# Optimization experiments

Hardware: AMD Instinct MI355X
Metric: run time of the kernel (lower is better)

The kernel has to match this reference:

```python
import jax, jax.numpy as jnp
import numpy as np

N = 50000   # nodes
E = 800000  # edges (before self-loops)
IN = 128    # input feature dim
H = 4       # attention heads


def setup_inputs() -> dict:
    key = jax.random.key(0)
    ks = jax.random.split(key, 32)
    f = lambda k, s: (jax.random.normal(k, s, dtype=jnp.float32) * 0.1)
    inp = {
        "x": jax.random.normal(ks[0], (N, IN), dtype=jnp.float32),
        "edge_index": jax.random.randint(ks[1], (2, E), 0, N, dtype=jnp.int32),
        "edge_attr": jax.random.normal(ks[2], (E, 1), dtype=jnp.float32),
        # GATConv 1: 128 -> 8 per head, 4 heads (concat -> 32)
        "W1": f(ks[3], (IN, 32)), "as1": f(ks[4], (H, 8)), "ad1": f(ks[5], (H, 8)), "b1": jnp.zeros((32,), jnp.float32),
        # GATConv 2: 32 -> 16 per head (concat -> 64)
        "W2": f(ks[6], (32, 64)), "as2": f(ks[7], (H, 16)), "ad2": f(ks[8], (H, 16)), "b2": jnp.zeros((64,), jnp.float32),
        # GATConv 3: 64 -> 32 per head (concat -> 128)
        "W3": f(ks[9], (64, 128)), "as3": f(ks[10], (H, 32)), "ad3": f(ks[11], (H, 32)), "b3": jnp.zeros((128,), jnp.float32),
        # GATConv 4: 128 -> 64 per head (concat -> 256)
        "W4": f(ks[12], (128, 256)), "as4": f(ks[13], (H, 64)), "ad4": f(ks[14], (H, 64)), "b4": jnp.zeros((256,), jnp.float32),
        # MLP head
        "Wr": f(ks[15], (256, 32)), "br": jnp.zeros((32,), jnp.float32),
        "Wf1": f(ks[16], (32, 64)), "bf1": jnp.zeros((64,), jnp.float32),
        "Wf2": f(ks[17], (64, 1)), "bf2": jnp.zeros((1,), jnp.float32),
    }
    return inp


def _gat_layer(x, W, a_src, a_dst, bias, src, dst):
    """PyG GATConv (concat=True, negative_slope=0.2, self-loops appended upstream)."""
    heads, C = a_src.shape
    h = (x @ W).reshape(-1, heads, C)              # [N, H, C]
    alpha_s = jnp.sum(h * a_src[None], axis=-1)    # [N, H]
    alpha_d = jnp.sum(h * a_dst[None], axis=-1)    # [N, H]
    e = jax.nn.leaky_relu(alpha_s[src] + alpha_d[dst], 0.2)  # [E', H]
    # segment softmax over incoming edges of each destination node
    emax = jax.ops.segment_max(e, dst, num_segments=N)
    ee = jnp.exp(e - emax[dst])
    denom = jax.ops.segment_sum(ee, dst, num_segments=N)
    alpha = ee / denom[dst]                        # [E', H]
    msg = h[src] * alpha[:, :, None]               # [E', H, C]
    out = jax.ops.segment_sum(msg, dst, num_segments=N)  # [N, H, C]
    return out.reshape(-1, heads * C) + bias


def reference(x, edge_index, edge_attr,
              W1, as1, ad1, b1, W2, as2, ad2, b2,
              W3, as3, ad3, b3, W4, as4, ad4, b4,
              Wr, br, Wf1, bf1, Wf2, bf2):
    # edge_attr is accepted but unused, matching the original forward.
    loop = jnp.arange(N, dtype=edge_index.dtype)
    src = jnp.concatenate([edge_index[0], loop])   # add self-loops (PyG default)
    dst = jnp.concatenate([edge_index[1], loop])
    h = jax.nn.elu(_gat_layer(x, W1, as1, ad1, b1, src, dst))
    h = jax.nn.elu(_gat_layer(h, W2, as2, ad2, b2, src, dst))
    h = jax.nn.elu(_gat_layer(h, W3, as3, ad3, b3, src, dst))
    h = jax.nn.elu(_gat_layer(h, W4, as4, ad4, b4, src, dst))
    h = jax.nn.elu(h @ Wr + br)
    h = jax.nn.elu(h @ Wf1 + bf1)
    return h @ Wf2 + bf2                           # [N, 1]
```

## Files before the change

kernel.cpp:

```cpp
#include <hip/hip_runtime.h>
#include <hip/hip_fp16.h>
#include <math.h>

constexpr int NN = 50000;
constexpr int NE = 800000;
constexpr int NEP = NE + NN;
constexpr int CAP = 96;
constexpr int SCAT_B = (NEP + 255) / 256;

typedef _Float16 half8_t __attribute__((ext_vector_type(8)));
typedef float    f32x4_t __attribute__((ext_vector_type(4)));

__device__ __forceinline__ float lrelu02(float x) { return x > 0.f ? x : 0.2f * x; }
__device__ __forceinline__ float eluf(float x)    { return x > 0.f ? x : (__expf(x) - 1.f); }
__device__ __forceinline__ float pick4(float4 q, int hd) {
  return (hd == 0) ? q.x : (hd == 1) ? q.y : (hd == 2) ? q.z : q.w;
}


__device__ __forceinline__ void pack_w_one(const float* __restrict__ W,
                                           __half* __restrict__ Wp,
                                           int M, int tid, int total) {
  if (tid >= total) return;
  int CT = M >> 4;
  int l = tid & 63;
  int c = (tid >> 6) % CT;
  int kc = (tid >> 6) / CT;
  int n = l & 15, q = l >> 4;
  __half* dst = Wp + (size_t)tid * 8;
  const float* src = W + (size_t)(kc * 32 + q * 8) * M + c * 16 + n;
  #pragma unroll
  for (int j = 0; j < 8; j++) dst[j] = __float2half_rn(src[j * M]);
}


__global__ __launch_bounds__(256) void scatter_pack_kernel(
    const int* __restrict__ edge_src, const int* __restrict__ edge_dst,
    int* __restrict__ count, int* __restrict__ csr_src,
    const float* __restrict__ W1, __half* __restrict__ Wp1,
    const float* __restrict__ W2, __half* __restrict__ Wp2,
    const float* __restrict__ W3, __half* __restrict__ Wp3,
    const float* __restrict__ W4, __half* __restrict__ Wp4,
    const float* __restrict__ Wr, __half* __restrict__ Wrp,
    const float* __restrict__ Wf1, __half* __restrict__ Wf1p) {
  int b = blockIdx.x;
  if (b < SCAT_B) {
    int i = b * 256 + threadIdx.x;
    if (i < NEP) {
      int s, d;
      if (i < NE) { s = edge_src[i]; d = edge_dst[i]; } else { s = i - NE; d = s; }
      int pos = atomicAdd(&count[d], 1);
      if (pos < CAP) csr_src[d * CAP + pos] = s;
    }
  } else {
    int tid = (b - SCAT_B) * 256 + threadIdx.x;
    if (tid < 512)            pack_w_one(W1, Wp1, 32,  tid,        512);
    else if (tid < 768)       pack_w_one(W2, Wp2, 64,  tid - 512,  256);
    else if (tid < 1792)      pack_w_one(W3, Wp3, 128, tid - 768,  1024);
    else if (tid < 5888)      pack_w_one(W4, Wp4, 256, tid - 1792, 4096);
    else if (tid < 6912)      pack_w_one(Wr, Wrp, 32,  tid - 5888, 1024);
    else if (tid < 7168)      pack_w_one(Wf1, Wf1p, 64, tid - 6912, 256);
  }
}


template<int M, int C, int CT>
__device__ __forceinline__ void alpha_epilogue(const f32x4_t* acc,
    const float* __restrict__ a_src, const float* __restrict__ a_dst,
    int row_base, int m, float* __restrict__ as_out, float* __restrict__ ad_out) {
  float aS[CT], aD[CT];
  #pragma unroll
  for (int c = 0; c < CT; c++) { aS[c] = a_src[c * 16 + m]; aD[c] = a_dst[c * 16 + m]; }

  if constexpr (C == 8) {
    #pragma unroll
    for (int r = 0; r < 4; r++) {
      float p0 = acc[0][r] * aS[0], p1 = acc[1][r] * aS[1];
      float q0 = acc[0][r] * aD[0], q1 = acc[1][r] * aD[1];
      #pragma unroll
      for (int off = 1; off < 8; off <<= 1) {
        p0 += __shfl_xor(p0, off); p1 += __shfl_xor(p1, off);
        q0 += __shfl_xor(q0, off); q1 += __shfl_xor(q1, off);
      }
      int row = row_base + r;
      if ((m & 7) == 0 && row < NN) {
        int hb = m >> 3;
        as_out[row * 4 + hb]     = p0;
        as_out[row * 4 + 2 + hb] = p1;
        ad_out[row * 4 + hb]     = q0;
        ad_out[row * 4 + 2 + hb] = q1;
      }
    }
  } else {
    constexpr int FPH = C / 16;
    #pragma unroll
    for (int r = 0; r < 4; r++) {
      float bs[4] = {0.f, 0.f, 0.f, 0.f}, bd[4] = {0.f, 0.f, 0.f, 0.f};
      #pragma unroll
      for (int c = 0; c < CT; c++) {
        int hd = c / FPH;
        bs[hd] += acc[c][r] * aS[c];
        bd[hd] += acc[c][r] * aD[c];
      }
      #pragma unroll
      for (int off = 1; off < 16; off <<= 1)
        #pragma unroll
        for (int h = 0; h < 4; h++) {
          bs[h] += __shfl_xor(bs[h], off);
          bd[h] += __shfl_xor(bd[h], off);
        }
      int row = row_base + r;
      if (m < 4 && row < NN) {
        float vs = (m == 0) ? bs[0] : (m == 1) ? bs[1] : (m == 2) ? bs[2] : bs[3];
        float vd = (m == 0) ? bd[0] : (m == 1) ? bd[1] : (m == 2) ? bd[2] : bd[3];
        as_out[row * 4 + m] = vs;
        ad_out[row * 4 + m] = vd;
      }
    }
  }
}


template<int M, int K, int C>
__global__ __launch_bounds__(256) void gemm_mfma_f32_kernel(const float* __restrict__ A,
    const __half* __restrict__ Wp, __half* __restrict__ Ch,
    const float* __restrict__ a_src, const float* __restrict__ a_dst,
    float* __restrict__ as_out, float* __restrict__ ad_out) {
  constexpr int CT = M / 16;
  constexpr int KC = K / 32;
  __shared__ _Float16 Ah[64 * 40];
  int t = threadIdx.x;
  int w = t >> 6, l = t & 63;
  int m = l & 15, q = l >> 4;
  int row0 = blockIdx.x * 64;

  f32x4_t acc[CT];
  #pragma unroll
  for (int c = 0; c < CT; c++) acc[c] = (f32x4_t){0.f, 0.f, 0.f, 0.f};

  const half8_t* Bfrag = (const half8_t*)Wp;

  for (int kc = 0; kc < KC; kc++) {
    __syncthreads();
    #pragma unroll
    for (int i = 0; i < 2; i++) {
      int idx = t + 256 * i;
      int row = idx >> 3, c4 = idx & 7;
      int gr = row0 + row; if (gr >= NN) gr = NN - 1;
      float4 v = *(const float4*)(A + (size_t)gr * K + kc * 32 + c4 * 4);
      _Float16 h[4] = {(_Float16)v.x, (_Float16)v.y, (_Float16)v.z, (_Float16)v.w};
      *(uint2*)(&Ah[row * 40 + c4 * 4]) = *(const uint2*)h;
    }
    __syncthreads();
    half8_t a = *(const half8_t*)(&Ah[(w * 16 + m) * 40 + q * 8]);
    #pragma unroll
    for (int c = 0; c < CT; c++) {
      half8_t b = Bfrag[(kc * CT + c) * 64 + l];
      acc[c] = __builtin_amdgcn_mfma_f32_16x16x32_f16(a, b, acc[c], 0, 0, 0);
    }
  }

  #pragma unroll
  for (int r = 0; r < 4; r++) {
    int row = row0 + w * 16 + q * 4 + r;
    if (row < NN) {
      #pragma unroll
      for (int c = 0; c < CT; c++)
        Ch[(size_t)row * M + c * 16 + m] = __float2half_rn(acc[c][r]);
    }
  }
  alpha_epilogue<M, C, CT>(acc, a_src, a_dst, row0 + w * 16 + q * 4, m, as_out, ad_out);
}


template<int M, int K, int C>
__global__ __launch_bounds__(256) void gemm_mfma_f16_kernel(const __half* __restrict__ A,
    const __half* __restrict__ Wp, __half* __restrict__ Ch,
    const float* __restrict__ a_src, const float* __restrict__ a_dst,
    float* __restrict__ as_out, float* __restrict__ ad_out) {
  constexpr int CT = M / 16;
  constexpr int KC = K / 32;
  __shared__ _Float16 Ah[64 * 40];
  int t = threadIdx.x;
  int w = t >> 6, l = t & 63;
  int m = l & 15, q = l >> 4;
  int row0 = blockIdx.x * 64;

  f32x4_t acc[CT];
  #pragma unroll
  for (int c = 0; c < CT; c++) acc[c] = (f32x4_t){0.f, 0.f, 0.f, 0.f};

  const half8_t* Bfrag = (const half8_t*)Wp;

  for (int kc = 0; kc < KC; kc++) {
    __syncthreads();
    {
      int row = t >> 2, c8 = t & 3;
      int gr = row0 + row; if (gr >= NN) gr = NN - 1;
      uint4 v = *(const uint4*)(A + (size_t)gr * K + kc * 32 + c8 * 8);
      *(uint4*)(&Ah[row * 40 + c8 * 8]) = v;
    }
    __syncthreads();
    half8_t a = *(const half8_t*)(&Ah[(w * 16 + m) * 40 + q * 8]);
    #pragma unroll
    for (int c = 0; c < CT; c++) {
      half8_t b = Bfrag[(kc * CT + c) * 64 + l];
      acc[c] = __builtin_amdgcn_mfma_f32_16x16x32_f16(a, b, acc[c], 0, 0, 0);
    }
  }

  #pragma unroll
  for (int r = 0; r < 4; r++) {
    int row = row0 + w * 16 + q * 4 + r;
    if (row < NN) {
      #pragma unroll
      for (int c = 0; c < CT; c++)
        Ch[(size_t)row * M + c * 16 + m] = __float2half_rn(acc[c][r]);
    }
  }
  alpha_epilogue<M, C, CT>(acc, a_src, a_dst, row0 + w * 16 + q * 4, m, as_out, ad_out);
}


template<int HC, int C>
__global__ __launch_bounds__(256) void agg_kernel(const __half* __restrict__ h,
    const float* __restrict__ as_v, const float* __restrict__ ad_v,
    const int* __restrict__ count, const int* __restrict__ csr_src,
    const float* __restrict__ bias, __half* __restrict__ out) {
  constexpr int V = HC / 8;
  constexpr int G = 64 / V;
  constexpr int P = 4;
  __shared__ float4 see4[4][CAP];
  __shared__ int    ssrc[4][CAP];
  int wid = threadIdx.x >> 6, lane = threadIdx.x & 63;
  int dst = blockIdx.x * 4 + wid;
  int base = dst * CAP;
  int deg = count[dst]; if (deg > CAP) deg = CAP;
  float4 ad = *(const float4*)(ad_v + dst * 4);

  float d0 = 0.f, d1 = 0.f, d2 = 0.f, d3 = 0.f;
  #pragma unroll
  for (int it = 0; it < 2; it++) {
    int j = lane + it * 64;
    if (j < deg) {
      int s = csr_src[base + j];
      float4 as = *(const float4*)(as_v + s * 4);
      float4 x = make_float4(__expf(lrelu02(as.x + ad.x)), __expf(lrelu02(as.y + ad.y)),
                             __expf(lrelu02(as.z + ad.z)), __expf(lrelu02(as.w + ad.w)));
      ssrc[wid][j] = s; see4[wid][j] = x;
      d0 += x.x; d1 += x.y; d2 += x.z; d3 += x.w;
    }
  }
  #pragma unroll
  for (int off = 32; off > 0; off >>= 1) {
    d0 += __shfl_xor(d0, off); d1 += __shfl_xor(d1, off);
    d2 += __shfl_xor(d2, off); d3 += __shfl_xor(d3, off);
  }
  float4 inv = make_float4(1.f / d0, 1.f / d1, 1.f / d2, 1.f / d3);

  int g = lane / V, v = lane % V;
  int hd = (v * 8) / C;
  float invh = pick4(inv, hd);
  int steps = (deg + G - 1) / G;
  const float4* hrows = (const float4*)h;

  float  px[P];
  float4 hv[P];
  #pragma unroll
  for (int k = 0; k < P; k++) {
    int jj = k * G + g;
    bool ok = jj < deg;
    int jc = ok ? jj : 0;
    int s = ssrc[wid][jc];
    float x = ((const float*)&see4[wid][jc])[hd];
    px[k] = ok ? x * invh : 0.f;
    hv[k] = hrows[(size_t)s * V + v];
  }

  float acc[8];
  #pragma unroll
  for (int i = 0; i < 8; i++) acc[i] = 0.f;
  int nB = (steps + P - 1) / P;
  for (int b = 1; b <= nB; b++) {
    #pragma unroll
    for (int k = 0; k < P; k++) {
      const __half2* hp = (const __half2*)&hv[k];
      float2 f0 = __half22float2(hp[0]);
      float2 f1 = __half22float2(hp[1]);
      float2 f2 = __half22float2(hp[2]);
      float2 f3 = __half22float2(hp[3]);
      float p = px[k];
      acc[0] += p * f0.x; acc[1] += p * f0.y;
      acc[2] += p * f1.x; acc[3] += p * f1.y;
      acc[4] += p * f2.x; acc[5] += p * f2.y;
      acc[6] += p * f3.x; acc[7] += p * f3.y;
      int jj = (b * P + k) * G + g;
      bool ok = jj < deg;
      int jc = ok ? jj : 0;
      int s = ssrc[wid][jc];
      float x = ((const float*)&see4[wid][jc])[hd];
      px[k] = ok ? x * invh : 0.f;
      hv[k] = hrows[(size_t)s * V + v];
    }
  }

  #pragma unroll
  for (int off = V; off < 64; off <<= 1)
    #pragma unroll
    for (int i = 0; i < 8; i++) acc[i] += __shfl_xor(acc[i], off);

  if (lane < V) {
    const float4* b4 = (const float4*)bias;
    float4 ba = b4[2 * v], bb = b4[2 * v + 1];
    _Float16 o[8];
    o[0] = (_Float16)eluf(acc[0] + ba.x); o[1] = (_Float16)eluf(acc[1] + ba.y);
    o[2] = (_Float16)eluf(acc[2] + ba.z); o[3] = (_Float16)eluf(acc[3] + ba.w);
    o[4] = (_Float16)eluf(acc[4] + bb.x); o[5] = (_Float16)eluf(acc[5] + bb.y);
    o[6] = (_Float16)eluf(acc[6] + bb.z); o[7] = (_Float16)eluf(acc[7] + bb.w);
    *(uint4*)(out + (size_t)dst * HC + v * 8) = *(const uint4*)o;
  }
}


__global__ __launch_bounds__(256) void mlp_mfma_kernel(const __half* __restrict__ h4,
    const __half* __restrict__ Wrp, const float* __restrict__ br,
    const __half* __restrict__ Wf1p, const float* __restrict__ bf1,
    const float* __restrict__ Wf2, const float* __restrict__ bf2,
    float* __restrict__ out) {
  __shared__ _Float16 rS[64 * 40];
  int t = threadIdx.x;
  int w = t >> 6, l = t & 63;
  int m = l & 15, q = l >> 4;
  int row0 = blockIdx.x * 64;
  const half8_t* Bwr  = (const half8_t*)Wrp;
  const half8_t* Bwf1 = (const half8_t*)Wf1p;

  int arow = row0 + w * 16 + m; if (arow >= NN) arow = NN - 1;
  const half8_t* Arow = (const half8_t*)(h4 + (size_t)arow * 256);
  half8_t afr[8];
  #pragma unroll
  for (int kc = 0; kc < 8; kc++) afr[kc] = Arow[kc * 4 + q];
  f32x4_t acc1[2];
  acc1[0] = (f32x4_t){0.f, 0.f, 0.f, 0.f};
  acc1[1] = (f32x4_t){0.f, 0.f, 0.f, 0.f};
  #pragma unroll
  for (int kc = 0; kc < 8; kc++) {
    acc1[0] = __builtin_amdgcn_mfma_f32_16x16x32_f16(afr[kc], Bwr[(kc * 2 + 0) * 64 + l], acc1[0], 0, 0, 0);
    acc1[1] = __builtin_amdgcn_mfma_f32_16x16x32_f16(afr[kc], Bwr[(kc * 2 + 1) * 64 + l], acc1[1], 0, 0, 0);
  }
  #pragma unroll
  for (int c = 0; c < 2; c++)
    #pragma unroll
    for (int r = 0; r < 4; r++) {
      float vv = eluf(acc1[c][r] + br[c * 16 + m]);
      rS[(w * 16 + q * 4 + r) * 40 + c * 16 + m] = (_Float16)vv;
    }
  __syncthreads();

  half8_t a2 = *(const half8_t*)(&rS[(w * 16 + m) * 40 + q * 8]);
  f32x4_t acc2[4];
  #pragma unroll
  for (int c = 0; c < 4; c++) acc2[c] = (f32x4_t){0.f, 0.f, 0.f, 0.f};
  #pragma unroll
  for (int c = 0; c < 4; c++)
    acc2[c] = __builtin_amdgcn_mfma_f32_16x16x32_f16(a2, Bwf1[c * 64 + l], acc2[c], 0, 0, 0);

  float wv[4] = {Wf2[m], Wf2[16 + m], Wf2[32 + m], Wf2[48 + m]};
  float rsum[4];
  #pragma unroll
  for (int r = 0; r < 4; r++) {
    float sr = 0.f;
    #pragma unroll
    for (int c = 0; c < 4; c++)
      sr += eluf(acc2[c][r] + bf1[c * 16 + m]) * wv[c];
    #pragma unroll
    for (int off = 1; off < 16; off <<= 1) sr += __shfl_xor(sr, off);
    rsum[r] = sr;
  }
  if (m == 0) {
    float b = bf2[0];
    #pragma unroll
    for (int r = 0; r < 4; r++) {
      int row = row0 + w * 16 + q * 4 + r;
      if (row < NN) out[row] = rsum[r] + b;
    }
  }
}


extern "C" void kernel_launch(void* const* d_in, const int* in_sizes, int n_in,
                              void* d_out, int out_size, void* d_ws, size_t ws_size,
                              hipStream_t stream) {
  const float* x   = (const float*)d_in[0];
  const int*   ei  = (const int*)d_in[1];
  const float* W1  = (const float*)d_in[3];
  const float* as1 = (const float*)d_in[4];
  const float* ad1 = (const float*)d_in[5];
  const float* b1  = (const float*)d_in[6];
  const float* W2  = (const float*)d_in[7];
  const float* as2 = (const float*)d_in[8];
  const float* ad2 = (const float*)d_in[9];
  const float* b2  = (const float*)d_in[10];
  const float* W3  = (const float*)d_in[11];
  const float* as3 = (const float*)d_in[12];
  const float* ad3 = (const float*)d_in[13];
  const float* b3  = (const float*)d_in[14];
  const float* W4  = (const float*)d_in[15];
  const float* as4 = (const float*)d_in[16];
  const float* ad4 = (const float*)d_in[17];
  const float* b4  = (const float*)d_in[18];
  const float* Wr  = (const float*)d_in[19];
  const float* br  = (const float*)d_in[20];
  const float* Wf1 = (const float*)d_in[21];
  const float* bf1 = (const float*)d_in[22];
  const float* Wf2 = (const float*)d_in[23];
  const float* bf2 = (const float*)d_in[24];
  float* out = (float*)d_out;

  char* p = (char*)d_ws;
  auto alloc = [&](size_t bytes) {
    char* q = p;
    p += (bytes + 255) & ~(size_t)255;
    return q;
  };
  int* count   = (int*)alloc((size_t)NN * 4);
  int* csr_src = (int*)alloc((size_t)NN * CAP * 4);
  __half* Hh = (__half*)alloc((size_t)NN * 256 * 2);
  __half* B2 = (__half*)alloc((size_t)NN * 128 * 2);
  __half* B3 = (__half*)alloc((size_t)NN * 256 * 2);
  float* as_buf = (float*)alloc((size_t)NN * 4 * 4);
  float* ad_buf = (float*)alloc((size_t)NN * 4 * 4);
  __half* Wp1 = (__half*)alloc((size_t)128 * 32 * 2);
  __half* Wp2 = (__half*)alloc((size_t)32 * 64 * 2);
  __half* Wp3 = (__half*)alloc((size_t)64 * 128 * 2);
  __half* Wp4 = (__half*)alloc((size_t)128 * 256 * 2);
  __half* Wrp = (__half*)alloc((size_t)256 * 32 * 2);
  __half* Wf1p = (__half*)alloc((size_t)32 * 64 * 2);

  const int* edge_src = ei;
  const int* edge_dst = ei + NE;

  hipMemsetAsync(count, 0, (size_t)NN * 4, stream);
  scatter_pack_kernel<<<SCAT_B + 28, 256, 0, stream>>>(
      edge_src, edge_dst, count, csr_src,
      W1, Wp1, W2, Wp2, W3, Wp3, W4, Wp4, Wr, Wrp, Wf1, Wf1p);

  int gb  = (NN + 63) / 64;
  int ggb = NN / 4;

  gemm_mfma_f32_kernel<32, 128, 8><<<gb, 256, 0, stream>>>(x, Wp1, Hh, as1, ad1, as_buf, ad_buf);
  agg_kernel<32, 8><<<ggb, 256, 0, stream>>>(Hh, as_buf, ad_buf, count, csr_src, b1, B2);

  gemm_mfma_f16_kernel<64, 32, 16><<<gb, 256, 0, stream>>>(B2, Wp2, Hh, as2, ad2, as_buf, ad_buf);
  agg_kernel<64, 16><<<ggb, 256, 0, stream>>>(Hh, as_buf, ad_buf, count, csr_src, b2, B3);

  gemm_mfma_f16_kernel<128, 64, 32><<<gb, 256, 0, stream>>>(B3, Wp3, Hh, as3, ad3, as_buf, ad_buf);
  agg_kernel<128, 32><<<ggb, 256, 0, stream>>>(Hh, as_buf, ad_buf, count, csr_src, b3, B2);

  gemm_mfma_f16_kernel<256, 128, 64><<<gb, 256, 0, stream>>>(B2, Wp4, Hh, as4, ad4, as_buf, ad_buf);
  agg_kernel<256, 64><<<ggb, 256, 0, stream>>>(Hh, as_buf, ad_buf, count, csr_src, b4, B3);

  mlp_mfma_kernel<<<gb, 256, 0, stream>>>(B3, Wrp, br, Wf1p, bf1, Wf2, bf2, out);
}
```

Measured before the change: 403.8 us.

## Fuse all GAT stages into one persistent cooperative kernel with grid syncs

```diff
diff --git a/kernel.cpp b/kernel.cpp
--- a/kernel.cpp
+++ b/kernel.cpp
@@ -1,12 +1,17 @@
 #include <hip/hip_runtime.h>
 #include <hip/hip_fp16.h>
+#include <hip/hip_cooperative_groups.h>
 #include <math.h>
+
+namespace cg = cooperative_groups;
 
 constexpr int NN = 50000;
 constexpr int NE = 800000;
 constexpr int NEP = NE + NN;
 constexpr int CAP = 96;
-constexpr int SCAT_B = (NEP + 255) / 256;
+constexpr int NT  = (NN + 63) / 64;
+constexpr int NQ  = NN / 4;
+constexpr int PACK_TOTAL = 7168;
 
 typedef _Float16 half8_t __attribute__((ext_vector_type(8)));
 typedef float    f32x4_t __attribute__((ext_vector_type(4)));
@@ -34,267 +39,203 @@
 }
 
 
-__global__ __launch_bounds__(256) void scatter_pack_kernel(
+__device__ __forceinline__ void zero_phase(int* __restrict__ count) {
+  for (int i = blockIdx.x * 256 + threadIdx.x; i < NN; i += gridDim.x * 256)
+    count[i] = 0;
+}
+
+
+__device__ __forceinline__ void scatter_pack_phase(
     const int* __restrict__ edge_src, const int* __restrict__ edge_dst,
     int* __restrict__ count, int* __restrict__ csr_src,
-    const float* __restrict__ W1, __half* __restrict__ Wp1,
-    const float* __restrict__ W2, __half* __restrict__ Wp2,
-    const float* __restrict__ W3, __half* __restrict__ Wp3,
-    const float* __restrict__ W4, __half* __restrict__ Wp4,
-    const float* __restrict__ Wr, __half* __restrict__ Wrp,
-    const float* __restrict__ Wf1, __half* __restrict__ Wf1p) {
-  int b = blockIdx.x;
-  if (b < SCAT_B) {
-    int i = b * 256 + threadIdx.x;
+    const float* W1, __half* Wp1, const float* W2, __half* Wp2,
+    const float* W3, __half* Wp3, const float* W4, __half* Wp4,
+    const float* Wr, __half* Wrp, const float* Wf1, __half* Wf1p) {
+  for (int i = blockIdx.x * 256 + threadIdx.x; i < NEP + PACK_TOTAL; i += gridDim.x * 256) {
     if (i < NEP) {
       int s, d;
       if (i < NE) { s = edge_src[i]; d = edge_dst[i]; } else { s = i - NE; d = s; }
       int pos = atomicAdd(&count[d], 1);
       if (pos < CAP) csr_src[d * CAP + pos] = s;
-    }
-  } else {
-    int tid = (b - SCAT_B) * 256 + threadIdx.x;
-    if (tid < 512)            pack_w_one(W1, Wp1, 32,  tid,        512);
-    else if (tid < 768)       pack_w_one(W2, Wp2, 64,  tid - 512,  256);
-    else if (tid < 1792)      pack_w_one(W3, Wp3, 128, tid - 768,  1024);
-    else if (tid < 5888)      pack_w_one(W4, Wp4, 256, tid - 1792, 4096);
-    else if (tid < 6912)      pack_w_one(Wr, Wrp, 32,  tid - 5888, 1024);
-    else if (tid < 7168)      pack_w_one(Wf1, Wf1p, 64, tid - 6912, 256);
+    } else {
+      int tid = i - NEP;
+      if (tid < 512)            pack_w_one(W1, Wp1, 32,  tid,        512);
+      else if (tid < 768)       pack_w_one(W2, Wp2, 64,  tid - 512,  256);
+      else if (tid < 1792)      pack_w_one(W3, Wp3, 128, tid - 768,  1024);
+      else if (tid < 5888)      pack_w_one(W4, Wp4, 256, tid - 1792, 4096);
+      else if (tid < 6912)      pack_w_one(Wr, Wrp, 32,  tid - 5888, 1024);
+      else                      pack_w_one(Wf1, Wf1p, 64, tid - 6912, 256);
+    }
   }
 }
 
 
-template<int M, int C, int CT>
-__device__ __forceinline__ void alpha_epilogue(const f32x4_t* acc,
-    const float* __restrict__ a_src, const float* __restrict__ a_dst,
-    int row_base, int m, float* __restrict__ as_out, float* __restrict__ ad_out) {
-  float aS[CT], aD[CT];
-  #pragma unroll
-  for (int c = 0; c < CT; c++) { aS[c] = a_src[c * 16 + m]; aD[c] = a_dst[c * 16 + m]; }
-
-  if constexpr (C == 8) {
-    #pragma unroll
-    for (int r = 0; r < 4; r++) {
-      float p0 = acc[0][r] * aS[0], p1 = acc[1][r] * aS[1];
-      float q0 = acc[0][r] * aD[0], q1 = acc[1][r] * aD[1];
-      #pragma unroll
-      for (int off = 1; off < 8; off <<= 1) {
-        p0 += __shfl_xor(p0, off); p1 += __shfl_xor(p1, off);
-        q0 += __shfl_xor(q0, off); q1 += __shfl_xor(q1, off);
-      }
-      int row = row_base + r;
-      if ((m & 7) == 0 && row < NN) {
-        int hb = m >> 3;
-        as_out[row * 4 + hb]     = p0;
-        as_out[row * 4 + 2 + hb] = p1;
-        ad_out[row * 4 + hb]     = q0;
-        ad_out[row * 4 + 2 + hb] = q1;
-      }
-    }
-  } else {
-    constexpr int FPH = C / 16;
-    #pragma unroll
-    for (int r = 0; r < 4; r++) {
-      float bs[4] = {0.f, 0.f, 0.f, 0.f}, bd[4] = {0.f, 0.f, 0.f, 0.f};
-      #pragma unroll
-      for (int c = 0; c < CT; c++) {
-        int hd = c / FPH;
-        bs[hd] += acc[c][r] * aS[c];
-        bd[hd] += acc[c][r] * aD[c];
-      }
-      #pragma unroll
-      for (int off = 1; off < 16; off <<= 1)
+template<int M, int K, int C, bool F32A>
+__device__ __forceinline__ void gemm_phase(const void* Av, const __half* __restrict__ Wp,
+    __half* __restrict__ Ch, const float* __restrict__ a_src, const float* __restrict__ a_dst,
+    float* __restrict__ as_out, float* __restrict__ ad_out, _Float16* Ah) {
+  constexpr int CT = M / 16;
+  constexpr int CHUNK = (CT > 8) ? 8 : CT;
+  constexpr int NCH = CT / CHUNK;
+  constexpr int KC = K / 32;
+  int t = threadIdx.x;
+  int w = t >> 6, l = t & 63, m = l & 15, q = l >> 4;
+  const half8_t* Bfrag = (const half8_t*)Wp;
+
+  for (int tile = blockIdx.x; tile < NT; tile += gridDim.x) {
+    int row0 = tile * 64;
+    #pragma unroll
+    for (int ch = 0; ch < NCH; ch++) {
+      f32x4_t acc[CHUNK];
+      #pragma unroll
+      for (int c = 0; c < CHUNK; c++) acc[c] = (f32x4_t){0.f, 0.f, 0.f, 0.f};
+      for (int kc = 0; kc < KC; kc++) {
+        __syncthreads();
+        if constexpr (F32A) {
+          const float* A = (const float*)Av;
+          #pragma unroll
+          for (int i = 0; i < 2; i++) {
+            int idx = t + 256 * i;
+            int row = idx >> 3, c4 = idx & 7;
+            int gr = row0 + row; if (gr >= NN) gr = NN - 1;
+            float4 vv = *(const float4*)(A + (size_t)gr * K + kc * 32 + c4 * 4);
+            _Float16 h4[4] = {(_Float16)vv.x, (_Float16)vv.y, (_Float16)vv.z, (_Float16)vv.w};
+            *(uint2*)(&Ah[row * 40 + c4 * 4]) = *(const uint2*)h4;
+          }
+        } else {
+          const __half* A = (const __half*)Av;
+          int row = t >> 2, c8 = t & 3;
+          int gr = row0 + row; if (gr >= NN) gr = NN - 1;
+          uint4 vv = *(const uint4*)(A + (size_t)gr * K + kc * 32 + c8 * 8);
+          *(uint4*)(&Ah[row * 40 + c8 * 8]) = vv;
+        }
+        __syncthreads();
+        half8_t a = *(const half8_t*)(&Ah[(w * 16 + m) * 40 + q * 8]);
         #pragma unroll
-        for (int h = 0; h < 4; h++) {
-          bs[h] += __shfl_xor(bs[h], off);
-          bd[h] += __shfl_xor(bd[h], off);
+        for (int c = 0; c < CHUNK; c++) {
+          half8_t b = Bfrag[(kc * CT + ch * CHUNK + c) * 64 + l];
+          acc[c] = __builtin_amdgcn_mfma_f32_16x16x32_f16(a, b, acc[c], 0, 0, 0);
         }
-      int row = row_base + r;
-      if (m < 4 && row < NN) {
-        float vs = (m == 0) ? bs[0] : (m == 1) ? bs[1] : (m == 2) ? bs[2] : bs[3];
-        float vd = (m == 0) ? bd[0] : (m == 1) ? bd[1] : (m == 2) ? bd[2] : bd[3];
-        as_out[row * 4 + m] = vs;
-        ad_out[row * 4 + m] = vd;
+      }
+      int rbase = row0 + w * 16 + q * 4;
+      #pragma unroll
+      for (int r = 0; r < 4; r++) {
+        int row = rbase + r;
+        if (row < NN) {
+          #pragma unroll
+          for (int c = 0; c < CHUNK; c++)
+            Ch[(size_t)row * M + (ch * CHUNK + c) * 16 + m] = __float2half_rn(acc[c][r]);
+        }
+      }
+      float aS[CHUNK], aD[CHUNK];
+      #pragma unroll
+      for (int c = 0; c < CHUNK; c++) {
+        int cg_ = ch * CHUNK + c;
+        aS[c] = a_src[cg_ * 16 + m];
+        aD[c] = a_dst[cg_ * 16 + m];
+      }
+      if constexpr (C == 8) {
+        #pragma unroll
+        for (int r = 0; r < 4; r++) {
+          float p0 = acc[0][r] * aS[0], p1 = acc[1][r] * aS[1];
+          float q0 = acc[0][r] * aD[0], q1 = acc[1][r] * aD[1];
+          #pragma unroll
+          for (int off = 1; off < 8; off <<= 1) {
+            p0 += __shfl_xor(p0, off); p1 += __shfl_xor(p1, off);
+            q0 += __shfl_xor(q0, off); q1 += __shfl_xor(q1, off);
+          }
+          int row = rbase + r;
+          if ((m & 7) == 0 && row < NN) {
+            int hb = m >> 3;
+            as_out[row * 4 + hb]     = p0;
+            as_out[row * 4 + 2 + hb] = p1;
+            ad_out[row * 4 + hb]     = q0;
+            ad_out[row * 4 + 2 + hb] = q1;
+          }
+        }
+      } else {
+        constexpr int FPH = C / 16;
+        constexpr int HPC = CHUNK / FPH;
+        int headBase = ch * HPC;
+        #pragma unroll
+        for (int r = 0; r < 4; r++) {
+          float bs[HPC], bd[HPC];
+          #pragma unroll
+          for (int hh = 0; hh < HPC; hh++) { bs[hh] = 0.f; bd[hh] = 0.f; }
+          #pragma unroll
+          for (int c = 0; c < CHUNK; c++) {
+            int hh = c / FPH;
+            bs[hh] += acc[c][r] * aS[c];
+            bd[hh] += acc[c][r] * aD[c];
+          }
+          #pragma unroll
+          for (int off = 1; off < 16; off <<= 1)
+            #pragma unroll
+            for (int hh = 0; hh < HPC; hh++) {
+              bs[hh] += __shfl_xor(bs[hh], off);
+              bd[hh] += __shfl_xor(bd[hh], off);
+            }
+          int row = rbase + r;
+          if (m < HPC && row < NN) {
+            float vs = bs[0], vd = bd[0];
+            #pragma unroll
+            for (int hh = 1; hh < HPC; hh++) if (m == hh) { vs = bs[hh]; vd = bd[hh]; }
+            as_out[row * 4 + headBase + m] = vs;
+            ad_out[row * 4 + headBase + m] = vd;
+          }
+        }
       }
     }
   }
 }
 
 
-template<int M, int K, int C>
-__global__ __launch_bounds__(256) void gemm_mfma_f32_kernel(const float* __restrict__ A,
-    const __half* __restrict__ Wp, __half* __restrict__ Ch,
-    const float* __restrict__ a_src, const float* __restrict__ a_dst,
-    float* __restrict__ as_out, float* __restrict__ ad_out) {
-  constexpr int CT = M / 16;
-  constexpr int KC = K / 32;
-  __shared__ _Float16 Ah[64 * 40];
-  int t = threadIdx.x;
-  int w = t >> 6, l = t & 63;
-  int m = l & 15, q = l >> 4;
-  int row0 = blockIdx.x * 64;
-
-  f32x4_t acc[CT];
-  #pragma unroll
-  for (int c = 0; c < CT; c++) acc[c] = (f32x4_t){0.f, 0.f, 0.f, 0.f};
-
-  const half8_t* Bfrag = (const half8_t*)Wp;
-
-  for (int kc = 0; kc < KC; kc++) {
-    __syncthreads();
-    #pragma unroll
-    for (int i = 0; i < 2; i++) {
-      int idx = t + 256 * i;
-      int row = idx >> 3, c4 = idx & 7;
-      int gr = row0 + row; if (gr >= NN) gr = NN - 1;
-      float4 v = *(const float4*)(A + (size_t)gr * K + kc * 32 + c4 * 4);
-      _Float16 h[4] = {(_Float16)v.x, (_Float16)v.y, (_Float16)v.z, (_Float16)v.w};
-      *(uint2*)(&Ah[row * 40 + c4 * 4]) = *(const uint2*)h;
-    }
-    __syncthreads();
-    half8_t a = *(const half8_t*)(&Ah[(w * 16 + m) * 40 + q * 8]);
-    #pragma unroll
-    for (int c = 0; c < CT; c++) {
-      half8_t b = Bfrag[(kc * CT + c) * 64 + l];
-      acc[c] = __builtin_amdgcn_mfma_f32_16x16x32_f16(a, b, acc[c], 0, 0, 0);
-    }
-  }
-
-  #pragma unroll
-  for (int r = 0; r < 4; r++) {
-    int row = row0 + w * 16 + q * 4 + r;
-    if (row < NN) {
-      #pragma unroll
-      for (int c = 0; c < CT; c++)
-        Ch[(size_t)row * M + c * 16 + m] = __float2half_rn(acc[c][r]);
-    }
-  }
-  alpha_epilogue<M, C, CT>(acc, a_src, a_dst, row0 + w * 16 + q * 4, m, as_out, ad_out);
-}
-
-
-template<int M, int K, int C>
-__global__ __launch_bounds__(256) void gemm_mfma_f16_kernel(const __half* __restrict__ A,
-    const __half* __restrict__ Wp, __half* __restrict__ Ch,
-    const float* __restrict__ a_src, const float* __restrict__ a_dst,
-    float* __restrict__ as_out, float* __restrict__ ad_out) {
-  constexpr int CT = M / 16;
-  constexpr int KC = K / 32;
-  __shared__ _Float16 Ah[64 * 40];
-  int t = threadIdx.x;
-  int w = t >> 6, l = t & 63;
-  int m = l & 15, q = l >> 4;
-  int row0 = blockIdx.x * 64;
-
-  f32x4_t acc[CT];
-  #pragma unroll
-  for (int c = 0; c < CT; c++) acc[c] = (f32x4_t){0.f, 0.f, 0.f, 0.f};
-
-  const half8_t* Bfrag = (const half8_t*)Wp;
-
-  for (int kc = 0; kc < KC; kc++) {
-    __syncthreads();
-    {
-      int row = t >> 2, c8 = t & 3;
-      int gr = row0 + row; if (gr >= NN) gr = NN - 1;
-      uint4 v = *(const uint4*)(A + (size_t)gr * K + kc * 32 + c8 * 8);
-      *(uint4*)(&Ah[row * 40 + c8 * 8]) = v;
-    }
-    __syncthreads();
-    half8_t a = *(const half8_t*)(&Ah[(w * 16 + m) * 40 + q * 8]);
-    #pragma unroll
-    for (int c = 0; c < CT; c++) {
-      half8_t b = Bfrag[(kc * CT + c) * 64 + l];
-      acc[c] = __builtin_amdgcn_mfma_f32_16x16x32_f16(a, b, acc[c], 0, 0, 0);
-    }
-  }
-
-  #pragma unroll
-  for (int r = 0; r < 4; r++) {
-    int row = row0 + w * 16 + q * 4 + r;
-    if (row < NN) {
-      #pragma unroll
-      for (int c = 0; c < CT; c++)
-        Ch[(size_t)row * M + c * 16 + m] = __float2half_rn(acc[c][r]);
-    }
-  }
-  alpha_epilogue<M, C, CT>(acc, a_src, a_dst, row0 + w * 16 + q * 4, m, as_out, ad_out);
-}
-
-
 template<int HC, int C>
-__global__ __launch_bounds__(256) void agg_kernel(const __half* __restrict__ h,
+__device__ __forceinline__ void agg_phase(const __half* __restrict__ h,
     const float* __restrict__ as_v, const float* __restrict__ ad_v,
     const int* __restrict__ count, const int* __restrict__ csr_src,
-    const float* __restrict__ bias, __half* __restrict__ out) {
+    const float* __restrict__ bias, __half* __restrict__ out,
+    float4 (*see4)[CAP], int (*ssrc)[CAP]) {
   constexpr int V = HC / 8;
   constexpr int G = 64 / V;
   constexpr int P = 4;
-  __shared__ float4 see4[4][CAP];
-  __shared__ int    ssrc[4][CAP];
   int wid = threadIdx.x >> 6, lane = threadIdx.x & 63;
-  int dst = blockIdx.x * 4 + wid;
-  int base = dst * CAP;
-  int deg = count[dst]; if (deg > CAP) deg = CAP;
-  float4 ad = *(const float4*)(ad_v + dst * 4);
-
-  float d0 = 0.f, d1 = 0.f, d2 = 0.f, d3 = 0.f;
-  #pragma unroll
-  for (int it = 0; it < 2; it++) {
-    int j = lane + it * 64;
-    if (j < deg) {
-      int s = csr_src[base + j];
-      float4 as = *(const float4*)(as_v + s * 4);
-      float4 x = make_float4(__expf(lrelu02(as.x + ad.x)), __expf(lrelu02(as.y + ad.y)),
-                             __expf(lrelu02(as.z + ad.z)), __expf(lrelu02(as.w + ad.w)));
-      ssrc[wid][j] = s; see4[wid][j] = x;
-      d0 += x.x; d1 += x.y; d2 += x.z; d3 += x.w;
-    }
-  }
-  #pragma unroll
-  for (int off = 32; off > 0; off >>= 1) {
-    d0 += __shfl_xor(d0, off); d1 += __shfl_xor(d1, off);
-    d2 += __shfl_xor(d2, off); d3 += __shfl_xor(d3, off);
-  }
-  float4 inv = make_float4(1.f / d0, 1.f / d1, 1.f / d2, 1.f / d3);
-
   int g = lane / V, v = lane % V;
   int hd = (v * 8) / C;
-  float invh = pick4(inv, hd);
-  int steps = (deg + G - 1) / G;
   const float4* hrows = (const float4*)h;
 
-  float  px[P];
-  float4 hv[P];
-  #pragma unroll
-  for (int k = 0; k < P; k++) {
-    int jj = k * G + g;
-    bool ok = jj < deg;
-    int jc = ok ? jj : 0;
-    int s = ssrc[wid][jc];
-    float x = ((const float*)&see4[wid][jc])[hd];
-    px[k] = ok ? x * invh : 0.f;
-    hv[k] = hrows[(size_t)s * V + v];
-  }
-
-  float acc[8];
-  #pragma unroll
-  for (int i = 0; i < 8; i++) acc[i] = 0.f;
-  int nB = (steps + P - 1) / P;
-  for (int b = 1; b <= nB; b++) {
+  for (int qd = blockIdx.x; qd < NQ; qd += gridDim.x) {
+    int dst = qd * 4 + wid;
+    int base = dst * CAP;
+    int deg = count[dst]; if (deg > CAP) deg = CAP;
+    float4 ad = *(const float4*)(ad_v + dst * 4);
+
+    float d0 = 0.f, d1 = 0.f, d2 = 0.f, d3 = 0.f;
+    #pragma unroll
+    for (int it = 0; it < 2; it++) {
+      int j = lane + it * 64;
+      if (j < deg) {
+        int s = csr_src[base + j];
+        float4 as = *(const float4*)(as_v + s * 4);
+        float4 x = make_float4(__expf(lrelu02(as.x + ad.x)), __expf(lrelu02(as.y + ad.y)),
+                               __expf(lrelu02(as.z + ad.z)), __expf(lrelu02(as.w + ad.w)));
+        ssrc[wid][j] = s; see4[wid][j] = x;
+        d0 += x.x; d1 += x.y; d2 += x.z; d3 += x.w;
+      }
+    }
+    #pragma unroll
+    for (int off = 32; off > 0; off >>= 1) {
+      d0 += __shfl_xor(d0, off); d1 += __shfl_xor(d1, off);
+      d2 += __shfl_xor(d2, off); d3 += __shfl_xor(d3, off);
+    }
+    float4 inv4 = make_float4(1.f / d0, 1.f / d1, 1.f / d2, 1.f / d3);
+    float invh = pick4(inv4, hd);
+
+    float  px[P];
+    float4 hv[P];
     #pragma unroll
     for (int k = 0; k < P; k++) {
-      const __half2* hp = (const __half2*)&hv[k];
-      float2 f0 = __half22float2(hp[0]);
-      float2 f1 = __half22float2(hp[1]);
-      float2 f2 = __half22float2(hp[2]);
-      float2 f3 = __half22float2(hp[3]);
-      float p = px[k];
-      acc[0] += p * f0.x; acc[1] += p * f0.y;
-      acc[2] += p * f1.x; acc[3] += p * f1.y;
-      acc[4] += p * f2.x; acc[5] += p * f2.y;
-      acc[6] += p * f3.x; acc[7] += p * f3.y;
-      int jj = (b * P + k) * G + g;
+      int jj = k * G + g;
       bool ok = jj < deg;
       int jc = ok ? jj : 0;
       int s = ssrc[wid][jc];
@@ -302,89 +243,189 @@
       px[k] = ok ? x * invh : 0.f;
       hv[k] = hrows[(size_t)s * V + v];
     }
+    float acc[8];
+    #pragma unroll
+    for (int i = 0; i < 8; i++) acc[i] = 0.f;
+    int steps = (deg + G - 1) / G;
+    int nB = (steps + P - 1) / P;
+    for (int b = 1; b <= nB; b++) {
+      #pragma unroll
+      for (int k = 0; k < P; k++) {
+        const __half2* hp = (const __half2*)&hv[k];
+        float2 f0 = __half22float2(hp[0]);
+        float2 f1 = __half22float2(hp[1]);
+        float2 f2 = __half22float2(hp[2]);
+        float2 f3 = __half22float2(hp[3]);
+        float p = px[k];
+        acc[0] += p * f0.x; acc[1] += p * f0.y;
+        acc[2] += p * f1.x; acc[3] += p * f1.y;
+        acc[4] += p * f2.x; acc[5] += p * f2.y;
+        acc[6] += p * f3.x; acc[7] += p * f3.y;
+        int jj = (b * P + k) * G + g;
+        bool ok = jj < deg;
+        int jc = ok ? jj : 0;
+        int s = ssrc[wid][jc];
+        float x = ((const float*)&see4[wid][jc])[hd];
+        px[k] = ok ? x * invh : 0.f;
+        hv[k] = hrows[(size_t)s * V + v];
+      }
+    }
+    #pragma unroll
+    for (int off = V; off < 64; off <<= 1)
+      #pragma unroll
+      for (int i = 0; i < 8; i++) acc[i] += __shfl_xor(acc[i], off);
+
+    if (lane < V) {
+      const float4* b4p = (const float4*)bias;
+      float4 ba = b4p[2 * v], bb = b4p[2 * v + 1];
+      _Float16 o[8];
+      o[0] = (_Float16)eluf(acc[0] + ba.x); o[1] = (_Float16)eluf(acc[1] + ba.y);
+      o[2] = (_Float16)eluf(acc[2] + ba.z); o[3] = (_Float16)eluf(acc[3] + ba.w);
+      o[4] = (_Float16)eluf(acc[4] + bb.x); o[5] = (_Float16)eluf(acc[5] + bb.y);
+      o[6] = (_Float16)eluf(acc[6] + bb.z); o[7] = (_Float16)eluf(acc[7] + bb.w);
+      *(uint4*)(out + (size_t)dst * HC + v * 8) = *(const uint4*)o;
+    }
   }
-
-  #pragma unroll
-  for (int off = V; off < 64; off <<= 1)
-    #pragma unroll
-    for (int i = 0; i < 8; i++) acc[i] += __shfl_xor(acc[i], off);
-
-  if (lane < V) {
-    const float4* b4 = (const float4*)bias;
-    float4 ba = b4[2 * v], bb = b4[2 * v + 1];
-    _Float16 o[8];
-    o[0] = (_Float16)eluf(acc[0] + ba.x); o[1] = (_Float16)eluf(acc[1] + ba.y);
-    o[2] = (_Float16)eluf(acc[2] + ba.z); o[3] = (_Float16)eluf(acc[3] + ba.w);
-    o[4] = (_Float16)eluf(acc[4] + bb.x); o[5] = (_Float16)eluf(acc[5] + bb.y);
-    o[6] = (_Float16)eluf(acc[6] + bb.z); o[7] = (_Float16)eluf(acc[7] + bb.w);
-    *(uint4*)(out + (size_t)dst * HC + v * 8) = *(const uint4*)o;
-  }
-}
-
-
-__global__ __launch_bounds__(256) void mlp_mfma_kernel(const __half* __restrict__ h4,
+}
+
+
+__device__ __forceinline__ void mlp_phase(const __half* __restrict__ h4,
     const __half* __restrict__ Wrp, const float* __restrict__ br,
     const __half* __restrict__ Wf1p, const float* __restrict__ bf1,
     const float* __restrict__ Wf2, const float* __restrict__ bf2,
-    float* __restrict__ out) {
-  __shared__ _Float16 rS[64 * 40];
+    float* __restrict__ out, _Float16* rS) {
   int t = threadIdx.x;
-  int w = t >> 6, l = t & 63;
-  int m = l & 15, q = l >> 4;
-  int row0 = blockIdx.x * 64;
+  int wid = t >> 6, l = t & 63, m = l & 15, q = l >> 4;
   const half8_t* Bwr  = (const half8_t*)Wrp;
   const half8_t* Bwf1 = (const half8_t*)Wf1p;
 
-  int arow = row0 + w * 16 + m; if (arow >= NN) arow = NN - 1;
-  const half8_t* Arow = (const half8_t*)(h4 + (size_t)arow * 256);
-  half8_t afr[8];
-  #pragma unroll
-  for (int kc = 0; kc < 8; kc++) afr[kc] = Arow[kc * 4 + q];
-  f32x4_t acc1[2];
-  acc1[0] = (f32x4_t){0.f, 0.f, 0.f, 0.f};
-  acc1[1] = (f32x4_t){0.f, 0.f, 0.f, 0.f};
-  #pragma unroll
-  for (int kc = 0; kc < 8; kc++) {
-    acc1[0] = __builtin_amdgcn_mfma_f32_16x16x32_f16(afr[kc], Bwr[(kc * 2 + 0) * 64 + l], acc1[0], 0, 0, 0);
-    acc1[1] = __builtin_amdgcn_mfma_f32_16x16x32_f16(afr[kc], Bwr[(kc * 2 + 1) * 64 + l], acc1[1], 0, 0, 0);
+  for (int tile = blockIdx.x; tile < NT; tile += gridDim.x) {
+    int row0 = tile * 64;
+    int arow = row0 + wid * 16 + m; if (arow >= NN) arow = NN - 1;
+    const half8_t* Arow = (const half8_t*)(h4 + (size_t)arow * 256);
+    half8_t afr[8];
+    #pragma unroll
+    for (int kc = 0; kc < 8; kc++) afr[kc] = Arow[kc * 4 + q];
+    f32x4_t acc1[2];
+    acc1[0] = (f32x4_t){0.f, 0.f, 0.f, 0.f};
+    acc1[1] = (f32x4_t){0.f, 0.f, 0.f, 0.f};
+    #pragma unroll
+    for (int kc = 0; kc < 8; kc++) {
+      acc1[0] = __builtin_amdgcn_mfma_f32_16x16x32_f16(afr[kc], Bwr[(kc * 2 + 0) * 64 + l], acc1[0], 0, 0, 0);
+      acc1[1] = __builtin_amdgcn_mfma_f32_16x16x32_f16(afr[kc], Bwr[(kc * 2 + 1) * 64 + l], acc1[1], 0, 0, 0);
+    }
+    __syncthreads();
+    #pragma unroll
+    for (int c = 0; c < 2; c++)
+      #pragma unroll
+      for (int r = 0; r < 4; r++) {
+        float vv = eluf(acc1[c][r] + br[c * 16 + m]);
+        rS[(wid * 16 + q * 4 + r) * 40 + c * 16 + m] = (_Float16)vv;
+      }
+    __syncthreads();
+
+    half8_t a2 = *(const half8_t*)(&rS[(wid * 16 + m) * 40 + q * 8]);
+    f32x4_t acc2[4];
+    #pragma unroll
+    for (int c = 0; c < 4; c++) acc2[c] = (f32x4_t){0.f, 0.f, 0.f, 0.f};
+    #pragma unroll
+    for (int c = 0; c < 4; c++)
+      acc2[c] = __builtin_amdgcn_mfma_f32_16x16x32_f16(a2, Bwf1[c * 64 + l], acc2[c], 0, 0, 0);
+
+    float wv[4] = {Wf2[m], Wf2[16 + m], Wf2[32 + m], Wf2[48 + m]};
+    float rsum[4];
+    #pragma unroll
+    for (int r = 0; r < 4; r++) {
+      float sr = 0.f;
+      #pragma unroll
+      for (int c = 0; c < 4; c++)
+        sr += eluf(acc2[c][r] + bf1[c * 16 + m]) * wv[c];
+      #pragma unroll
+      for (int off = 1; off < 16; off <<= 1) sr += __shfl_xor(sr, off);
+      rsum[r] = sr;
+    }
+    if (m == 0) {
+      float b = bf2[0];
+      #pragma unroll
+      for (int r = 0; r < 4; r++) {
+        int row = row0 + wid * 16 + q * 4 + r;
+        if (row < NN) out[row] = rsum[r] + b;
+      }
+    }
   }
-  #pragma unroll
-  for (int c = 0; c < 2; c++)
-    #pragma unroll
-    for (int r = 0; r < 4; r++) {
-      float vv = eluf(acc1[c][r] + br[c * 16 + m]);
-      rS[(w * 16 + q * 4 + r) * 40 + c * 16 + m] = (_Float16)vv;
-    }
-  __syncthreads();
-
-  half8_t a2 = *(const half8_t*)(&rS[(w * 16 + m) * 40 + q * 8]);
-  f32x4_t acc2[4];
-  #pragma unroll
-  for (int c = 0; c < 4; c++) acc2[c] = (f32x4_t){0.f, 0.f, 0.f, 0.f};
-  #pragma unroll
-  for (int c = 0; c < 4; c++)
-    acc2[c] = __builtin_amdgcn_mfma_f32_16x16x32_f16(a2, Bwf1[c * 64 + l], acc2[c], 0, 0, 0);
-
-  float wv[4] = {Wf2[m], Wf2[16 + m], Wf2[32 + m], Wf2[48 + m]};
-  float rsum[4];
-  #pragma unroll
-  for (int r = 0; r < 4; r++) {
-    float sr = 0.f;
-    #pragma unroll
-    for (int c = 0; c < 4; c++)
-      sr += eluf(acc2[c][r] + bf1[c * 16 + m]) * wv[c];
-    #pragma unroll
-    for (int off = 1; off < 16; off <<= 1) sr += __shfl_xor(sr, off);
-    rsum[r] = sr;
-  }
-  if (m == 0) {
-    float b = bf2[0];
-    #pragma unroll
-    for (int r = 0; r < 4; r++) {
-      int row = row0 + w * 16 + q * 4 + r;
-      if (row < NN) out[row] = rsum[r] + b;
-    }
-  }
+}
+
+
+struct MegaParams {
+  const float* x; const int* edge_src; const int* edge_dst;
+  const float *W1, *as1, *ad1, *b1;
+  const float *W2, *as2, *ad2, *b2;
+  const float *W3, *as3, *ad3, *b3;
+  const float *W4, *as4, *ad4, *b4;
+  const float *Wr, *br, *Wf1, *bf1, *Wf2, *bf2;
+  float* out;
+  int* count; int* csr_src;
+  __half *bufA, *bufB;
+  float *as_b, *ad_b;
+  __half *Wp1, *Wp2, *Wp3, *Wp4, *Wrp, *Wf1p;
+};
+
+__global__ __launch_bounds__(256, 5) void mega_kernel(MegaParams P) {
+  cg::grid_group grid = cg::this_grid();
+  __shared__ __align__(16) char smem[7680];
+  float4 (*see4)[CAP] = (float4 (*)[CAP])smem;
+  int    (*ssrc)[CAP] = (int (*)[CAP])(smem + 6144);
+  _Float16* Ah = (_Float16*)smem;
+
+  zero_phase(P.count);
+  grid.sync();
+  scatter_pack_phase(P.edge_src, P.edge_dst, P.count, P.csr_src,
+                     P.W1, P.Wp1, P.W2, P.Wp2, P.W3, P.Wp3, P.W4, P.Wp4,
+                     P.Wr, P.Wrp, P.Wf1, P.Wf1p);
+  grid.sync();
+  gemm_phase<32, 128, 8, true>(P.x, P.Wp1, P.bufA, P.as1, P.ad1, P.as_b, P.ad_b, Ah);
+  grid.sync();
+  agg_phase<32, 8>(P.bufA, P.as_b, P.ad_b, P.count, P.csr_src, P.b1, P.bufB, see4, ssrc);
+  grid.sync();
+  gemm_phase<64, 32, 16, false>(P.bufB, P.Wp2, P.bufA, P.as2, P.ad2, P.as_b, P.ad_b, Ah);
+  grid.sync();
+  agg_phase<64, 16>(P.bufA, P.as_b, P.ad_b, P.count, P.csr_src, P.b2, P.bufB, see4, ssrc);
+  grid.sync();
+  gemm_phase<128, 64, 32, false>(P.bufB, P.Wp3, P.bufA, P.as3, P.ad3, P.as_b, P.ad_b, Ah);
+  grid.sync();
+  agg_phase<128, 32>(P.bufA, P.as_b, P.ad_b, P.count, P.csr_src, P.b3, P.bufB, see4, ssrc);
+  grid.sync();
+  gemm_phase<256, 128, 64, false>(P.bufB, P.Wp4, P.bufA, P.as4, P.ad4, P.as_b, P.ad_b, Ah);
+  grid.sync();
+  agg_phase<256, 64>(P.bufA, P.as_b, P.ad_b, P.count, P.csr_src, P.b4, P.bufB, see4, ssrc);
+  grid.sync();
+  mlp_phase(P.bufB, P.Wrp, P.br, P.Wf1p, P.bf1, P.Wf2, P.bf2, P.out, Ah);
+}
+
+
+__global__ __launch_bounds__(256) void zero_wrap(MegaParams P) { zero_phase(P.count); }
+__global__ __launch_bounds__(256) void scat_wrap(MegaParams P) {
+  scatter_pack_phase(P.edge_src, P.edge_dst, P.count, P.csr_src,
+                     P.W1, P.Wp1, P.W2, P.Wp2, P.W3, P.Wp3, P.W4, P.Wp4,
+                     P.Wr, P.Wrp, P.Wf1, P.Wf1p);
+}
+template<int M, int K, int C, bool F32A>
+__global__ __launch_bounds__(256) void gemm_wrap(MegaParams P, const void* A, __half* Ch,
+    const float* a_src, const float* a_dst) {
+  __shared__ __align__(16) _Float16 Ah[64 * 40];
+  gemm_phase<M, K, C, F32A>(A, (M == 32) ? P.Wp1 : (M == 64) ? P.Wp2 : (M == 128) ? P.Wp3 : P.Wp4,
+                            Ch, a_src, a_dst, P.as_b, P.ad_b, Ah);
+}
+template<int HC, int C>
+__global__ __launch_bounds__(256) void agg_wrap(MegaParams P, const __half* h,
+    const float* bias, __half* out) {
+  __shared__ __align__(16) char sm[7680];
+  agg_phase<HC, C>(h, P.as_b, P.ad_b, P.count, P.csr_src, bias, out,
+                   (float4 (*)[CAP])sm, (int (*)[CAP])(sm + 6144));
+}
+__global__ __launch_bounds__(256) void mlp_wrap(MegaParams P) {
+  __shared__ __align__(16) _Float16 rS[64 * 40];
+  mlp_phase(P.bufB, P.Wrp, P.br, P.Wf1p, P.bf1, P.Wf2, P.bf2, P.out, rS);
 }
 
 
@@ -393,29 +434,22 @@
                               hipStream_t stream) {
   const float* x   = (const float*)d_in[0];
   const int*   ei  = (const int*)d_in[1];
-  const float* W1  = (const float*)d_in[3];
-  const float* as1 = (const float*)d_in[4];
-  const float* ad1 = (const float*)d_in[5];
-  const float* b1  = (const float*)d_in[6];
-  const float* W2  = (const float*)d_in[7];
-  const float* as2 = (const float*)d_in[8];
-  const float* ad2 = (const float*)d_in[9];
-  const float* b2  = (const float*)d_in[10];
-  const float* W3  = (const float*)d_in[11];
-  const float* as3 = (const float*)d_in[12];
-  const float* ad3 = (const float*)d_in[13];
-  const float* b3  = (const float*)d_in[14];
-  const float* W4  = (const float*)d_in[15];
-  const float* as4 = (const float*)d_in[16];
-  const float* ad4 = (const float*)d_in[17];
-  const float* b4  = (const float*)d_in[18];
-  const float* Wr  = (const float*)d_in[19];
-  const float* br  = (const float*)d_in[20];
-  const float* Wf1 = (const float*)d_in[21];
-  const float* bf1 = (const float*)d_in[22];
-  const float* Wf2 = (const float*)d_in[23];
-  const float* bf2 = (const float*)d_in[24];
-  float* out = (float*)d_out;
+  MegaParams P;
+  P.x = x;
+  P.edge_src = ei;
+  P.edge_dst = ei + NE;
+  P.W1 = (const float*)d_in[3];  P.as1 = (const float*)d_in[4];
+  P.ad1 = (const float*)d_in[5]; P.b1 = (const float*)d_in[6];
+  P.W2 = (const float*)d_in[7];  P.as2 = (const float*)d_in[8];
+  P.ad2 = (const float*)d_in[9]; P.b2 = (const float*)d_in[10];
+  P.W3 = (const float*)d_in[11]; P.as3 = (const float*)d_in[12];
+  P.ad3 = (const float*)d_in[13]; P.b3 = (const float*)d_in[14];
+  P.W4 = (const float*)d_in[15]; P.as4 = (const float*)d_in[16];
+  P.ad4 = (const float*)d_in[17]; P.b4 = (const float*)d_in[18];
+  P.Wr = (const float*)d_in[19]; P.br = (const float*)d_in[20];
+  P.Wf1 = (const float*)d_in[21]; P.bf1 = (const float*)d_in[22];
+  P.Wf2 = (const float*)d_in[23]; P.bf2 = (const float*)d_in[24];
+  P.out = (float*)d_out;
 
   char* p = (char*)d_ws;
   auto alloc = [&](size_t bytes) {
@@ -423,42 +457,43 @@
     p += (bytes + 255) & ~(size_t)255;
     return q;
   };
-  int* count   = (int*)alloc((size_t)NN * 4);
-  int* csr_src = (int*)alloc((size_t)NN * CAP * 4);
-  __half* Hh = (__half*)alloc((size_t)NN * 256 * 2);
-  __half* B2 = (__half*)alloc((size_t)NN * 128 * 2);
-  __half* B3 = (__half*)alloc((size_t)NN * 256 * 2);
-  float* as_buf = (float*)alloc((size_t)NN * 4 * 4);
-  float* ad_buf = (float*)alloc((size_t)NN * 4 * 4);
-  __half* Wp1 = (__half*)alloc((size_t)128 * 32 * 2);
-  __half* Wp2 = (__half*)alloc((size_t)32 * 64 * 2);
-  __half* Wp3 = (__half*)alloc((size_t)64 * 128 * 2);
-  __half* Wp4 = (__half*)alloc((size_t)128 * 256 * 2);
-  __half* Wrp = (__half*)alloc((size_t)256 * 32 * 2);
-  __half* Wf1p = (__half*)alloc((size_t)32 * 64 * 2);
-
-  const int* edge_src = ei;
-  const int* edge_dst = ei + NE;
-
-  hipMemsetAsync(count, 0, (size_t)NN * 4, stream);
-  scatter_pack_kernel<<<SCAT_B + 28, 256, 0, stream>>>(
-      edge_src, edge_dst, count, csr_src,
-      W1, Wp1, W2, Wp2, W3, Wp3, W4, Wp4, Wr, Wrp, Wf1, Wf1p);
-
-  int gb  = (NN + 63) / 64;
-  int ggb = NN / 4;
-
-  gemm_mfma_f32_kernel<32, 128, 8><<<gb, 256, 0, stream>>>(x, Wp1, Hh, as1, ad1, as_buf, ad_buf);
-  agg_kernel<32, 8><<<ggb, 256, 0, stream>>>(Hh, as_buf, ad_buf, count, csr_src, b1, B2);
-
-  gemm_mfma_f16_kernel<64, 32, 16><<<gb, 256, 0, stream>>>(B2, Wp2, Hh, as2, ad2, as_buf, ad_buf);
-  agg_kernel<64, 16><<<ggb, 256, 0, stream>>>(Hh, as_buf, ad_buf, count, csr_src, b2, B3);
-
-  gemm_mfma_f16_kernel<128, 64, 32><<<gb, 256, 0, stream>>>(B3, Wp3, Hh, as3, ad3, as_buf, ad_buf);
-  agg_kernel<128, 32><<<ggb, 256, 0, stream>>>(Hh, as_buf, ad_buf, count, csr_src, b3, B2);
-
-  gemm_mfma_f16_kernel<256, 128, 64><<<gb, 256, 0, stream>>>(B2, Wp4, Hh, as4, ad4, as_buf, ad_buf);
-  agg_kernel<256, 64><<<ggb, 256, 0, stream>>>(Hh, as_buf, ad_buf, count, csr_src, b4, B3);
-
-  mlp_mfma_kernel<<<gb, 256, 0, stream>>>(B3, Wrp, br, Wf1p, bf1, Wf2, bf2, out);
-}
+  P.count   = (int*)alloc((size_t)NN * 4);
+  P.csr_src = (int*)alloc((size_t)NN * CAP * 4);
+  P.bufA = (__half*)alloc((size_t)NN * 256 * 2);
+  P.bufB = (__half*)alloc((size_t)NN * 256 * 2);
+  P.as_b = (float*)alloc((size_t)NN * 4 * 4);
+  P.ad_b = (float*)alloc((size_t)NN * 4 * 4);
+  P.Wp1 = (__half*)alloc((size_t)128 * 32 * 2);
+  P.Wp2 = (__half*)alloc((size_t)32 * 64 * 2);
+  P.Wp3 = (__half*)alloc((size_t)64 * 128 * 2);
+  P.Wp4 = (__half*)alloc((size_t)128 * 256 * 2);
+  P.Wrp = (__half*)alloc((size_t)256 * 32 * 2);
+  P.Wf1p = (__half*)alloc((size_t)32 * 64 * 2);
+
+  int occ = 0;
+  hipError_t qe = hipOccupancyMaxActiveBlocksPerMultiprocessor(
+      &occ, reinterpret_cast<const void*>(mega_kernel), 256, 0);
+  if (qe != hipSuccess || occ < 1) occ = 4;
+  if (occ > 8) occ = 8;
+  int grid = occ * 256;
+
+  void* kargs[] = { (void*)&P };
+  hipError_t le = hipLaunchCooperativeKernel(
+      reinterpret_cast<const void*>(mega_kernel), dim3(grid), dim3(256),
+      kargs, 0, stream);
+
+  if (le != hipSuccess) {
+    int scg = (NEP + PACK_TOTAL + 255) / 256;
+    zero_wrap<<<(NN + 255) / 256, 256, 0, stream>>>(P);
+    scat_wrap<<<scg, 256, 0, stream>>>(P);
+    gemm_wrap<32, 128, 8, true><<<NT, 256, 0, stream>>>(P, P.x, P.bufA, P.as1, P.ad1);
+    agg_wrap<32, 8><<<NQ, 256, 0, stream>>>(P, P.bufA, P.b1, P.bufB);
+    gemm_wrap<64, 32, 16, false><<<NT, 256, 0, stream>>>(P, P.bufB, P.bufA, P.as2, P.ad2);
+    agg_wrap<64, 16><<<NQ, 256, 0, stream>>>(P, P.bufA, P.b2, P.bufB);
+    gemm_wrap<128, 64, 32, false><<<NT, 256, 0, stream>>>(P, P.bufB, P.bufA, P.as3, P.ad3);
+    agg_wrap<128, 32><<<NQ, 256, 0, stream>>>(P, P.bufA, P.b3, P.bufB);
+    gemm_wrap<256, 128, 64, false><<<NT, 256, 0, stream>>>(P, P.bufB, P.bufA, P.as4, P.ad4);
+    agg_wrap<256, 64><<<NQ, 256, 0, stream>>>(P, P.bufA, P.b4, P.bufB);
+    mlp_wrap<<<NT, 256, 0, stream>>>(P);
+  }
+}
```

After: 1.251 ms. 210% more time.
